# Performance work log

Hardware: AMD Instinct MI355X
Metric: run time of the kernel (lower is better)

Reference implementation:

```python
import jax, jax.numpy as jnp
import numpy as np

D_MODEL = 32
D_INNER = 64
D_STATE = 16
D_CONV = 4
DT_RANK = 2  # ceil(d_model/16)
ADJUST = 0.5
EPS = 1e-5


def _conv2d(x, w, b, pad):
    y = jax.lax.conv_general_dilated(x, w, (1, 1), [(pad, pad), (pad, pad)],
                                     dimension_numbers=('NCHW', 'OIHW', 'NCHW'))
    return y + b[None, :, None, None]


def _bn(x, g, be, m, v):
    # eval-mode BatchNorm2d
    return (x - m[None, :, None, None]) / jnp.sqrt(v + EPS)[None, :, None, None] \
        * g[None, :, None, None] + be[None, :, None, None]


def _cbr(x, w, b, g, be, m, v, pad):
    return jax.nn.relu(_bn(_conv2d(x, w, b, pad), g, be, m, v))


def _ln_tokens(p, g, b):
    # p: (B,1,H,W); LayerNorm(1) over the singleton channel per token
    B, _, H, W = p.shape
    t = p.reshape(B, 1, H * W).transpose(0, 2, 1)  # (B,N,1)
    mu = t.mean(-1, keepdims=True)
    var = ((t - mu) ** 2).mean(-1, keepdims=True)
    t = (t - mu) / jnp.sqrt(var + EPS) * g + b
    return t.transpose(0, 2, 1).reshape(B, 1, H, W)


def _selective_scan(u, delta, A, Bm, Cm, Dp):
    # u, delta: (B,L,d_inner); Bm, Cm: (B,L,d_state)
    dBu = delta * u
    def step(h, inp):
        d_t, bu_t, B_t, C_t = inp  # (B,di),(B,di),(B,ds),(B,ds)
        dA = jnp.exp(d_t[..., None] * A)        # (B,di,ds)
        h = dA * h + bu_t[..., None] * B_t[:, None, :]
        y = jnp.einsum('bds,bs->bd', h, C_t)
        return h, y
    h0 = jnp.zeros((u.shape[0], D_INNER, D_STATE), u.dtype)
    xs = (delta.transpose(1, 0, 2), dBu.transpose(1, 0, 2),
          Bm.transpose(1, 0, 2), Cm.transpose(1, 0, 2))
    _, ys = jax.lax.scan(step, h0, xs)
    return ys.transpose(1, 0, 2) + u * Dp


def _mamba(tok, in_w, cw, cb, xp_w, dt_w, dt_b, A_log, Dp, out_w):
    # tok: (B,L,d_model)
    xz = tok @ in_w.T                              # (B,L,2*d_inner)
    xm, z = xz[..., :D_INNER], xz[..., D_INNER:]
    # causal depthwise conv1d over sequence
    xc = jax.lax.conv_general_dilated(xm.transpose(0, 2, 1), cw, (1,), [(D_CONV - 1, 0)],
                                      dimension_numbers=('NCH', 'OIH', 'NCH'),
                                      feature_group_count=D_INNER)
    u = jax.nn.silu(xc + cb[None, :, None]).transpose(0, 2, 1)  # (B,L,di)
    xdbl = u @ xp_w.T                              # (B,L,dt_rank+2*d_state)
    dt = xdbl[..., :DT_RANK]
    Bm = xdbl[..., DT_RANK:DT_RANK + D_STATE]
    Cm = xdbl[..., DT_RANK + D_STATE:]
    delta = jax.nn.softplus(dt @ dt_w.T + dt_b)    # (B,L,di)
    A = -jnp.exp(A_log)                            # (di,ds)
    y = _selective_scan(u, delta, A, Bm, Cm, Dp)
    y = y * jax.nn.silu(z)
    return y @ out_w.T


def hpe_forward(x, w7, b7, g1, be1, m1, v1, w3, b3, g2, be2, m2, v2,
                w1, b1, g3, be3, m3, v3,
                in_w, cw, cb, xp_w, dt_w, dt_b, A_log, Dp, out_w,
                w4, b4, g4, be4, m4, v4, p1w, p1b, p2w, p2b, lng, lnb):
    B, C, H, W = x.shape
    x = x.reshape(B, C, H // 2, 2, W // 2, 2).max(axis=(3, 5))  # MaxPool2d(2,2)
    x = _cbr(x, w7, b7, g1, be1, m1, v1, 3)
    x = _cbr(x, w3, b3, g2, be2, m2, v2, 1)
    x = _cbr(x, w1, b1, g3, be3, m3, v3, 0)
    B, C, H, W = x.shape
    p1 = _ln_tokens(_conv2d(x, p1w, p1b, 0), lng, lnb)
    tok = x.reshape(B, C, H * W).transpose(0, 2, 1)  # (B,N,C)
    y = _mamba(tok, in_w, cw, cb, xp_w, dt_w, dt_b, A_log, Dp, out_w)
    x = ADJUST * y.transpose(0, 2, 1).reshape(B, C, H, W) + (1.0 - ADJUST) * x
    p2 = _ln_tokens(_conv2d(x, p2w, p2b, 0), lng, lnb)
    return _cbr(x, w4, b4, g4, be4, m4, v4, 0) + p1 + p2


def setup_inputs() -> dict:
    key = jax.random.key(0)
    ks = jax.random.split(key, 16)
    f32 = jnp.float32
    def nrm(k, s, sc=0.05):
        return jax.random.normal(k, s, dtype=f32) * sc
    C = 32
    d = {}
    d['x'] = jax.random.normal(ks[0], (8, 3, 256, 256), dtype=f32)
    d['w7'] = nrm(ks[1], (C, 3, 7, 7), 0.1); d['b7'] = jnp.zeros(C, f32)
    d['g1'] = jnp.ones(C, f32); d['be1'] = jnp.zeros(C, f32); d['m1'] = jnp.zeros(C, f32); d['v1'] = jnp.ones(C, f32)
    d['w3'] = nrm(ks[2], (C, C, 3, 3), 0.1); d['b3'] = jnp.zeros(C, f32)
    d['g2'] = jnp.ones(C, f32); d['be2'] = jnp.zeros(C, f32); d['m2'] = jnp.zeros(C, f32); d['v2'] = jnp.ones(C, f32)
    d['w1'] = nrm(ks[3], (C, C, 1, 1), 0.2); d['b1'] = jnp.zeros(C, f32)
    d['g3'] = jnp.ones(C, f32); d['be3'] = jnp.zeros(C, f32); d['m3'] = jnp.zeros(C, f32); d['v3'] = jnp.ones(C, f32)
    d['in_w'] = nrm(ks[4], (2 * D_INNER, C), 0.1)
    d['cw'] = nrm(ks[5], (D_INNER, 1, D_CONV), 0.2); d['cb'] = jnp.zeros(D_INNER, f32)
    d['xp_w'] = nrm(ks[6], (DT_RANK + 2 * D_STATE, D_INNER), 0.1)
    d['dt_w'] = nrm(ks[7], (D_INNER, DT_RANK), 0.5)
    d['dt_b'] = jnp.log(jnp.expm1(jnp.linspace(0.001, 0.1, D_INNER, dtype=f32)))
    d['A_log'] = jnp.log(jnp.tile(jnp.arange(1, D_STATE + 1, dtype=f32), (D_INNER, 1)))
    d['Dp'] = jnp.ones(D_INNER, f32)
    d['out_w'] = nrm(ks[8], (C, D_INNER), 0.1)
    d['w4'] = nrm(ks[9], (C, C, 1, 1), 0.2); d['b4'] = jnp.zeros(C, f32)
    d['g4'] = jnp.ones(C, f32); d['be4'] = jnp.zeros(C, f32); d['m4'] = jnp.zeros(C, f32); d['v4'] = jnp.ones(C, f32)
    d['p1w'] = nrm(ks[10], (1, C, 1, 1), 0.2); d['p1b'] = jnp.zeros(1, f32)
    d['p2w'] = nrm(ks[11], (1, C, 1, 1), 0.2); d['p2b'] = jnp.zeros(1, f32)
    d['lng'] = jnp.ones(1, f32); d['lnb'] = nrm(ks[12], (1,), 1.0)
    return d


def reference(x, w7, b7, g1, be1, m1, v1, w3, b3, g2, be2, m2, v2,
              w1, b1, g3, be3, m3, v3,
              in_w, cw, cb, xp_w, dt_w, dt_b, A_log, Dp, out_w,
              w4, b4, g4, be4, m4, v4, p1w, p1b, p2w, p2b, lng, lnb):
    return hpe_forward(x, w7, b7, g1, be1, m1, v1, w3, b3, g2, be2, m2, v2,
                       w1, b1, g3, be3, m3, v3,
                       in_w, cw, cb, xp_w, dt_w, dt_b, A_log, Dp, out_w,
                       w4, b4, g4, be4, m4, v4, p1w, p1b, p2w, p2b, lng, lnb)
```

## Files before the change

### kernel.cpp

```cpp
#include <hip/hip_runtime.h>
#include <hip/hip_bf16.h>

#define B_ 8
#define HP 128
#define WP 128
#define LL 16384
#define NC 512
#define LC 32
#define NSUP 32
#define KSUP 16
#define EPSF 1e-5f
#define LOG2E 1.44269504f

__device__ __forceinline__ float softplusf(float x){
    float ax = fabsf(x);
    float e = exp2f(-LOG2E*ax);
    return fmaxf(x, 0.f) + 0.69314718f*log2f(1.f + e);
}
__device__ __forceinline__ float siluf(float x){
    return x * __builtin_amdgcn_rcpf(1.f + exp2f(-LOG2E*x));
}

__global__ void prep_kernel(const float* __restrict__ w7, const float* __restrict__ b7,
                            const float* __restrict__ g1, const float* __restrict__ be1,
                            const float* __restrict__ m1, const float* __restrict__ v1,
                            const float* __restrict__ w3, const float* __restrict__ b3,
                            const float* __restrict__ g2, const float* __restrict__ be2,
                            const float* __restrict__ m2, const float* __restrict__ v2,
                            const float* __restrict__ w1, const float* __restrict__ b1,
                            const float* __restrict__ g3, const float* __restrict__ be3,
                            const float* __restrict__ m3, const float* __restrict__ v3,
                            const float* __restrict__ w4, const float* __restrict__ b4,
                            const float* __restrict__ g4, const float* __restrict__ be4,
                            const float* __restrict__ m4, const float* __restrict__ v4,
                            const float* __restrict__ out_w,
                            float* __restrict__ w7t, float* __restrict__ bf1,
                            float* __restrict__ w3t, float* __restrict__ bf2,
                            float* __restrict__ w1t, float* __restrict__ bf3,
                            float* __restrict__ w4t, float* __restrict__ bf4,
                            float* __restrict__ WcT, float* __restrict__ w4h){
    int tid = threadIdx.x;
    if (tid < 32){
        float s1 = g1[tid]*rsqrtf(v1[tid]+EPSF);
        bf1[tid] = (b7[tid]-m1[tid])*s1 + be1[tid];
        float s2 = g2[tid]*rsqrtf(v2[tid]+EPSF);
        bf2[tid] = (b3[tid]-m2[tid])*s2 + be2[tid];
        float s3 = g3[tid]*rsqrtf(v3[tid]+EPSF);
        bf3[tid] = (b1[tid]-m3[tid])*s3 + be3[tid];
        float s4 = g4[tid]*rsqrtf(v4[tid]+EPSF);
        bf4[tid] = (b4[tid]-m4[tid])*s4 + be4[tid];
    }
    for (int e = tid; e < 147*32; e += blockDim.x){
        int co = e & 31; int r = e >> 5;
        float s = g1[co]*rsqrtf(v1[co]+EPSF);
        w7t[e] = w7[co*147 + r]*s;
    }
    for (int e = tid; e < 288*32; e += blockDim.x){
        int co = e & 31; int r = e >> 5;
        float s = g2[co]*rsqrtf(v2[co]+EPSF);
        w3t[e] = w3[co*288 + r]*s;
    }
    for (int e = tid; e < 32*32; e += blockDim.x){
        int co = e & 31; int ci = e >> 5;
        float s3 = g3[co]*rsqrtf(v3[co]+EPSF);
        w1t[e] = w1[co*32+ci]*s3;
        float s4 = g4[co]*rsqrtf(v4[co]+EPSF);
        w4t[e] = w4[co*32+ci]*s4;
    }
    __syncthreads();
    for (int e = tid; e < 64*32; e += blockDim.x){
        int co = e & 31; int d = e >> 5;
        float a = 0.f;
        for (int c = 0; c < 32; c++) a = fmaf(w4t[c*32+co], out_w[c*64+d], a);
        WcT[d*32+co] = 0.5f*a;
    }
    for (int e = tid; e < 1024; e += blockDim.x) w4h[e] = 0.5f*w4t[e];
}

__global__ __launch_bounds__(256) void pool_kernel(const float* __restrict__ x, float* __restrict__ p){
    int idx = blockIdx.x*256 + threadIdx.x;
    if (idx >= B_*3*HP*WP) return;
    int j = idx & 127; int i = (idx>>7) & 127; int bc = idx >> 14;
    const float* src = x + ((size_t)bc*256 + 2*i)*256 + 2*j;
    float a = src[0], b = src[1], c = src[256], d = src[257];
    p[idx] = fmaxf(fmaxf(a,b), fmaxf(c,d));
}

__global__ __launch_bounds__(256) void conv7_kernel(const float* __restrict__ p, const float* __restrict__ w7t,
                                                    const float* __restrict__ bf1, float* __restrict__ x1){
    __shared__ float lds[3*10*70];
    int tx = threadIdx.x & 63, ty = threadIdx.x >> 6;
    int b = blockIdx.z >> 1, coh = (blockIdx.z & 1) * 16;
    int i0 = blockIdx.y*4, j0 = blockIdx.x*64;
    for (int e = threadIdx.x; e < 3*10*70; e += 256){
        int col = e % 70; int r2 = e / 70; int row = r2 % 10; int ci = r2 / 10;
        int gi = i0 + row - 3, gj = j0 + col - 3;
        float v = 0.f;
        if (gi>=0 && gi<HP && gj>=0 && gj<WP)
            v = p[((b*3+ci)*HP+gi)*WP+gj];
        lds[e] = v;
    }
    __syncthreads();
    float acc[16];
    #pragma unroll
    for (int co=0; co<16; co++) acc[co]=0.f;
    for (int ci=0; ci<3; ci++){
        for (int ky=0; ky<7; ky++){
            #pragma unroll
            for (int kx=0; kx<7; kx++){
                float v = lds[ci*700 + (ty+ky)*70 + tx+kx];
                const float* w = w7t + ((ci*7+ky)*7+kx)*32 + coh;
                #pragma unroll
                for (int co=0; co<16; co++) acc[co] = fmaf(v, w[co], acc[co]);
            }
        }
    }
    size_t base = ((size_t)(b*32)+coh)*LL + (i0+ty)*WP + (j0+tx);
    #pragma unroll
    for (int co=0; co<16; co++)
        x1[base + (size_t)co*LL] = fmaxf(acc[co]+bf1[coh+co], 0.f);
}

__global__ __launch_bounds__(256) void conv31_kernel(const float* __restrict__ x1, const float* __restrict__ w3t,
                                                     const float* __restrict__ bf2, const float* __restrict__ w1t,
                                                     const float* __restrict__ bf3, float* __restrict__ x3){
    __shared__ float lds[16*6*66];
    int tx = threadIdx.x & 63, ty = threadIdx.x >> 6;
    int b = blockIdx.z;
    int i0 = blockIdx.y*4, j0 = blockIdx.x*64;
    float acc[32];
    #pragma unroll
    for (int co=0; co<32; co++) acc[co]=0.f;
    for (int pass=0; pass<2; ++pass){
        int cibase = pass*16;
        for (int e = threadIdx.x; e < 16*6*66; e += 256){
            int col = e % 66; int r2 = e / 66; int row = r2 % 6; int ci = r2 / 6;
            int gi = i0 + row - 1, gj = j0 + col - 1;
            float v = 0.f;
            if (gi>=0 && gi<HP && gj>=0 && gj<WP)
                v = x1[((b*32+cibase+ci)*HP+gi)*WP+gj];
            lds[e] = v;
        }
        __syncthreads();
        for (int ci=0; ci<16; ci++){
            #pragma unroll
            for (int ky=0; ky<3; ky++){
                #pragma unroll
                for (int kx=0; kx<3; kx++){
                    float v = lds[ci*396 + (ty+ky)*66 + tx+kx];
                    const float* w = w3t + (((cibase+ci)*3+ky)*3+kx)*32;
                    #pragma unroll
                    for (int co=0; co<32; co++) acc[co] = fmaf(v, w[co], acc[co]);
                }
            }
        }
        __syncthreads();
    }
    #pragma unroll
    for (int co=0; co<32; co++) acc[co] = fmaxf(acc[co]+bf2[co], 0.f);
    float a3[32];
    #pragma unroll
    for (int co=0; co<32; co++) a3[co] = bf3[co];
    #pragma unroll
    for (int ci=0; ci<32; ci++){
        float v = acc[ci];
        const float* w = w1t + ci*32;
        #pragma unroll
        for (int co=0; co<32; co++) a3[co] = fmaf(v, w[co], a3[co]);
    }
    size_t base = ((size_t)(b*32))*LL + (i0+ty)*WP + (j0+tx);
    #pragma unroll
    for (int co=0; co<32; co++)
        x3[base + (size_t)co*LL] = fmaxf(a3[co], 0.f);
}

__global__ __launch_bounds__(256) void inproj_dw_kernel(const float* __restrict__ x3, const float* __restrict__ in_w,
                                                        const float* __restrict__ cw, const float* __restrict__ cb,
                                                        const float* __restrict__ xp_w,
                                                        float* __restrict__ Z, float* __restrict__ U,
                                                        float* __restrict__ BC, float* __restrict__ CC,
                                                        float* __restrict__ DT){
    __shared__ float xmL[67*65];
    __shared__ float buf[64*65];
    int lane = threadIdx.x & 63;
    int wv = __builtin_amdgcn_readfirstlane(threadIdx.x >> 6);
    int b = blockIdx.x >> 8;
    int t0 = (blockIdx.x & 255) * 64;
    size_t gbase = (size_t)b*LL + t0;

    float xvm[32], xvz[32];
    int tm = t0 - 3 + lane;
    #pragma unroll
    for (int c=0;c<32;c++)
        xvm[c] = (tm >= 0) ? x3[((size_t)(b*32+c))*LL + tm] : 0.f;
    #pragma unroll
    for (int c=0;c<32;c++)
        xvz[c] = x3[((size_t)(b*32+c))*LL + t0 + lane];

    for (int kk=0; kk<16; ++kk){
        int k = wv*16 + kk;
        const float* wxp = in_w + k*32;
        const float* wzp = in_w + (64+k)*32;
        float am = 0.f, az = 0.f;
        #pragma unroll
        for (int c=0;c<32;c++){
            am = fmaf(xvm[c], wxp[c], am);
            az = fmaf(xvz[c], wzp[c], az);
        }
        xmL[lane*65 + k] = am;
        buf[lane*65 + k] = az;
        if (lane >= 61){
            float am2 = 0.f;
            #pragma unroll
            for (int c=0;c<32;c++) am2 = fmaf(xvz[c], wxp[c], am2);
            xmL[(lane+3)*65 + k] = am2;
        }
    }
    __syncthreads();
    for (int i=0;i<16;i++){
        int tt = wv*16 + i;
        Z[(gbase + tt)*64 + lane] = buf[tt*65 + lane];
    }
    __syncthreads();
    for (int kk=0; kk<16; ++kk){
        int k = wv*16 + kk;
        float c0 = cw[k*4], c1 = cw[k*4+1], c2 = cw[k*4+2], c3 = cw[k*4+3];
        float a = cb[k];
        a = fmaf(c0, xmL[(lane+0)*65 + k], a);
        a = fmaf(c1, xmL[(lane+1)*65 + k], a);
        a = fmaf(c2, xmL[(lane+2)*65 + k], a);
        a = fmaf(c3, xmL[(lane+3)*65 + k], a);
        buf[lane*65 + k] = siluf(a);
    }
    __syncthreads();
    for (int i=0;i<16;i++){
        int tt = wv*16 + i;
        U[(gbase + tt)*64 + lane] = buf[tt*65 + lane];
    }
    {
        float* oT = xmL;
        const float* urow = &buf[lane*65];
        float a[9];
        #pragma unroll
        for (int jj=0;jj<9;jj++) a[jj]=0.f;
        #pragma unroll
        for (int dc=0; dc<4; ++dc){
            float uv[16];
            #pragma unroll
            for (int i=0;i<16;i++) uv[i] = urow[dc*16+i];
            #pragma unroll
            for (int jj=0;jj<9;jj++){
                int j = wv*9+jj; if (j>33) j=33;
                const float* w = xp_w + j*64 + dc*16;
                float s = 0.f;
                #pragma unroll
                for (int i=0;i<16;i++) s = fmaf(uv[i], w[i], s);
                a[jj] += s;
            }
        }
        #pragma unroll
        for (int jj=0;jj<9;jj++){
            int j = wv*9+jj;
            if (j < 34) oT[lane*35 + j] = a[jj];
        }
    }
    __syncthreads();
    {
        const float* oT = xmL;
        int e = threadIdx.x;
        if (e < 128){
            int tk = e >> 1, j = e & 1;
            DT[(gbase + tk)*2 + j] = oT[tk*35 + j];
        }
        for (int it=0; it<4; ++it){
            int e2 = threadIdx.x + it*256;
            int tk = e2 >> 4, j = e2 & 15;
            BC[(gbase + tk)*16 + j] = oT[tk*35 + 2 + j];
            CC[(gbase + tk)*16 + j] = oT[tk*35 + 18 + j];
        }
    }
}

__global__ __launch_bounds__(256) void scan1_kernel(const float* __restrict__ DT, const float* __restrict__ U,
                                                    const float* __restrict__ BC,
                                                    const float* __restrict__ dt_w, const float* __restrict__ dt_b,
                                                    const float* __restrict__ A_log,
                                                    float* __restrict__ HEND, float* __restrict__ SDL){
    int d = threadIdx.x & 63; int cq = threadIdx.x >> 6;
    int b = blockIdx.x >> 7; int c = ((blockIdx.x & 127) << 2) | cq;
    float A2_0 = -__expf(A_log[d*16])*LOG2E;
    float w0 = dt_w[d*2], w1 = dt_w[d*2+1], bD = dt_b[d];
    float h[16];
    #pragma unroll
    for (int s=0;s<16;s++) h[s]=0.f;
    float sd = 0.f;
    size_t tbase = (size_t)b*LL + c*LC;
    const float2* dtp = (const float2*)(DT + tbase*2);
    const float* up = U + tbase*64 + d;
    const float4* bp = (const float4*)(BC + tbase*16);
    for (int tt=0; tt<LC; ++tt){
        float2 dv = dtp[tt];
        float delta = softplusf(fmaf(dv.x, w0, fmaf(dv.y, w1, bD)));
        float uv = up[(size_t)tt*64];
        float du = delta*uv;
        float4 B0 = bp[tt*4+0], B1 = bp[tt*4+1], B2 = bp[tt*4+2], B3 = bp[tt*4+3];
        float bb[16] = {B0.x,B0.y,B0.z,B0.w, B1.x,B1.y,B1.z,B1.w,
                        B2.x,B2.y,B2.z,B2.w, B3.x,B3.y,B3.z,B3.w};
        float a1 = exp2f(delta*A2_0);
        float a2=a1*a1, a3=a2*a1, a4=a2*a2;
        float a8=a4*a4, a12=a8*a4, a16=a8*a8;
        float rr[16] = {a1,a2,a3,a4, a4*a1,a4*a2,a4*a3,a8,
                        a8*a1,a8*a2,a8*a3,a12, a12*a1,a12*a2,a12*a3,a16};
        #pragma unroll
        for (int s=0;s<16;s++)
            h[s] = fmaf(rr[s], h[s], du*bb[s]);
        sd += delta;
    }
    float4* hp = (float4*)(HEND + (((size_t)(b*NC)+c)*64 + d)*16);
    hp[0] = make_float4(h[0],h[1],h[2],h[3]);
    hp[1] = make_float4(h[4],h[5],h[6],h[7]);
    hp[2] = make_float4(h[8],h[9],h[10],h[11]);
    hp[3] = make_float4(h[12],h[13],h[14],h[15]);
    SDL[((size_t)(b*NC)+c)*64 + d] = sd;
}

__global__ __launch_bounds__(256) void scan2a_kernel(const float* __restrict__ HEND, const float* __restrict__ SDL,
                                                     const float* __restrict__ A_log,
                                                     float* __restrict__ HSUP, float* __restrict__ SDS){
    int tid = blockIdx.x*256 + threadIdx.x;
    int s = tid & 15; int d = (tid>>4) & 63; int g = (tid>>10) & 31; int b = tid >> 15;
    float A2 = -__expf(A_log[d*16+s])*LOG2E;
    float H = 0.f, sds = 0.f;
    #pragma unroll 4
    for (int k=0; k<KSUP; ++k){
        int c = g*KSUP + k;
        size_t ci = ((size_t)(b*NC)+c)*64 + d;
        float sv = SDL[ci];
        H = fmaf(exp2f(A2*sv), H, HEND[ci*16+s]);
        sds += sv;
    }
    HSUP[tid] = H;
    if (s == 0) SDS[(b*NSUP+g)*64 + d] = sds;
}

__global__ __launch_bounds__(256) void scan2b_kernel(float* __restrict__ HSUP, const float* __restrict__ SDS,
                                                     const float* __restrict__ A_log){
    int tid = blockIdx.x*256 + threadIdx.x;
    if (tid >= B_*64*16) return;
    int s = tid & 15; int d = (tid>>4) & 63; int b = tid >> 10;
    float A2 = -__expf(A_log[d*16+s])*LOG2E;
    float H = 0.f;
    for (int g=0; g<NSUP; ++g){
        size_t idx = ((((size_t)b*NSUP+g)*64 + d)*16) + s;
        float tmp = HSUP[idx];
        HSUP[idx] = H;
        H = fmaf(exp2f(A2*SDS[(b*NSUP+g)*64 + d]), H, tmp);
    }
}

__global__ __launch_bounds__(256) void scan2c_kernel(float* __restrict__ HEND, const float* __restrict__ SDL,
                                                     const float* __restrict__ A_log,
                                                     const float* __restrict__ HSUP){
    int tid = blockIdx.x*256 + threadIdx.x;
    int s = tid & 15; int d = (tid>>4) & 63; int g = (tid>>10) & 31; int b = tid >> 15;
    float A2 = -__expf(A_log[d*16+s])*LOG2E;
    float H = HSUP[tid];
    #pragma unroll 4
    for (int k=0; k<KSUP; ++k){
        int c = g*KSUP + k;
        size_t ci = ((size_t)(b*NC)+c)*64 + d;
        float tmp = HEND[ci*16+s];
        HEND[ci*16+s] = H;
        H = fmaf(exp2f(A2*SDL[ci]), H, tmp);
    }
}

__global__ __launch_bounds__(256) void scan3_kernel(const float* __restrict__ DT, const float* __restrict__ U,
                                                    const float* __restrict__ BC, const float* __restrict__ CC,
                                                    const float* __restrict__ dt_w, const float* __restrict__ dt_b,
                                                    const float* __restrict__ A_log, const float* __restrict__ Dp,
                                                    const float* __restrict__ HST, const float* __restrict__ Z,
                                                    const float* __restrict__ WcT, const float* __restrict__ w4h,
                                                    const float* __restrict__ x3, const float* __restrict__ bf4,
                                                    const float* __restrict__ lnb, float* __restrict__ out){
    __shared__ float yT[128*65];
    __shared__ float wl[97*32];
    int d = threadIdx.x & 63; int cq = threadIdx.x >> 6;
    int b = blockIdx.x >> 7; int cbase4 = (blockIdx.x & 127) << 2;
    int c = cbase4 | cq;
    for (int e = threadIdx.x; e < 3072; e += 256)
        wl[e] = (e < 2048) ? WcT[e] : w4h[e-2048];
    if (threadIdx.x < 32) wl[3072+threadIdx.x] = bf4[threadIdx.x];
    int tok = threadIdx.x & 127;
    int hf  = threadIdx.x >> 7;
    size_t tcol = (size_t)cbase4*LC + tok;
    float x3v[32];
    #pragma unroll
    for (int c2=0;c2<32;c2++) x3v[c2] = x3[((size_t)(b*32+c2))*LL + tcol];

    float A2_0 = -__expf(A_log[d*16])*LOG2E;
    float w0 = dt_w[d*2], w1 = dt_w[d*2+1], bD = dt_b[d];
    float Dd = Dp[d];
    float h[16];
    const float4* hp = (const float4*)(HST + (((size_t)(b*NC)+c)*64 + d)*16);
    #pragma unroll
    for (int q=0;q<4;q++){
        float4 f = hp[q];
        h[q*4]=f.x; h[q*4+1]=f.y; h[q*4+2]=f.z; h[q*4+3]=f.w;
    }
    size_t tbase = (size_t)b*LL + c*LC;
    const float2* dtp = (const float2*)(DT + tbase*2);
    const float* up = U + tbase*64 + d;
    const float4* bp = (const float4*)(BC + tbase*16);
    const float4* cp = (const float4*)(CC + tbase*16);
    const float* zp = Z + tbase*64 + d;
    for (int tt=0; tt<LC; ++tt){
        float2 dv = dtp[tt];
        float delta = softplusf(fmaf(dv.x, w0, fmaf(dv.y, w1, bD)));
        float uv = up[(size_t)tt*64];
        float du = delta*uv;
        float4 B0 = bp[tt*4+0], B1 = bp[tt*4+1], B2 = bp[tt*4+2], B3 = bp[tt*4+3];
        float4 C0 = cp[tt*4+0], C1 = cp[tt*4+1], C2 = cp[tt*4+2], C3 = cp[tt*4+3];
        float bb[16] = {B0.x,B0.y,B0.z,B0.w, B1.x,B1.y,B1.z,B1.w,
                        B2.x,B2.y,B2.z,B2.w, B3.x,B3.y,B3.z,B3.w};
        float cc[16] = {C0.x,C0.y,C0.z,C0.w, C1.x,C1.y,C1.z,C1.w,
                        C2.x,C2.y,C2.z,C2.w, C3.x,C3.y,C3.z,C3.w};
        float a1 = exp2f(delta*A2_0);
        float a2=a1*a1, a3=a2*a1, a4=a2*a2;
        float a8=a4*a4, a12=a8*a4, a16=a8*a8;
        float rr[16] = {a1,a2,a3,a4, a4*a1,a4*a2,a4*a3,a8,
                        a8*a1,a8*a2,a8*a3,a12, a12*a1,a12*a2,a12*a3,a16};
        float y0=0.f, y1=0.f, y2=0.f, y3=0.f;
        #pragma unroll
        for (int s=0;s<4;s++){
            h[s]    = fmaf(rr[s],    h[s],    du*bb[s]);
            h[s+4]  = fmaf(rr[s+4],  h[s+4],  du*bb[s+4]);
            h[s+8]  = fmaf(rr[s+8],  h[s+8],  du*bb[s+8]);
            h[s+12] = fmaf(rr[s+12], h[s+12], du*bb[s+12]);
            y0 = fmaf(h[s],    cc[s],    y0);
            y1 = fmaf(h[s+4],  cc[s+4],  y1);
            y2 = fmaf(h[s+8],  cc[s+8],  y2);
            y3 = fmaf(h[s+12], cc[s+12], y3);
        }
        float y = (y0+y1)+(y2+y3);
        float zv = zp[(size_t)tt*64];
        float yy = fmaf(uv, Dd, y);
        yT[(cq*LC + tt)*65 + d] = yy * siluf(zv);
    }
    __syncthreads();
    int cob = hf*16;
    const float* yrow = &yT[tok*65];
    float acc[16];
    #pragma unroll
    for (int o=0;o<16;o++) acc[o] = wl[3072+cob+o];
    #pragma unroll
    for (int dc=0; dc<4; ++dc){
        float uv[16];
        #pragma unroll
        for (int i=0;i<16;i++) uv[i] = yrow[dc*16+i];
        #pragma unroll
        for (int i=0;i<16;i++){
            const float* w = &wl[(dc*16+i)*32 + cob];
            float v = uv[i];
            #pragma unroll
            for (int o=0;o<16;o++) acc[o] = fmaf(v, w[o], acc[o]);
        }
    }
    #pragma unroll
    for (int c2=0; c2<32; ++c2){
        float v = x3v[c2];
        const float* w = &wl[(64+c2)*32 + cob];
        #pragma unroll
        for (int o=0;o<16;o++) acc[o] = fmaf(v, w[o], acc[o]);
    }
    float add2 = 2.f*lnb[0];
    #pragma unroll
    for (int o=0;o<16;o++)
        out[((size_t)(b*32)+cob+o)*LL + tcol] = fmaxf(acc[o], 0.f) + add2;
}

extern "C" void kernel_launch(void* const* d_in, const int* in_sizes, int n_in,
                              void* d_out, int out_size, void* d_ws, size_t ws_size,
                              hipStream_t stream) {
    const float* x    = (const float*)d_in[0];
    const float* w7   = (const float*)d_in[1];
    const float* b7   = (const float*)d_in[2];
    const float* g1   = (const float*)d_in[3];
    const float* be1  = (const float*)d_in[4];
    const float* m1   = (const float*)d_in[5];
    const float* v1   = (const float*)d_in[6];
    const float* w3   = (const float*)d_in[7];
    const float* b3   = (const float*)d_in[8];
    const float* g2   = (const float*)d_in[9];
    const float* be2  = (const float*)d_in[10];
    const float* m2   = (const float*)d_in[11];
    const float* v2   = (const float*)d_in[12];
    const float* w1   = (const float*)d_in[13];
    const float* b1   = (const float*)d_in[14];
    const float* g3   = (const float*)d_in[15];
    const float* be3  = (const float*)d_in[16];
    const float* m3   = (const float*)d_in[17];
    const float* v3   = (const float*)d_in[18];
    const float* in_w = (const float*)d_in[19];
    const float* cw   = (const float*)d_in[20];
    const float* cb   = (const float*)d_in[21];
    const float* xp_w = (const float*)d_in[22];
    const float* dt_w = (const float*)d_in[23];
    const float* dt_b = (const float*)d_in[24];
    const float* A_log= (const float*)d_in[25];
    const float* Dp   = (const float*)d_in[26];
    const float* out_w= (const float*)d_in[27];
    const float* w4   = (const float*)d_in[28];
    const float* b4   = (const float*)d_in[29];
    const float* g4   = (const float*)d_in[30];
    const float* be4  = (const float*)d_in[31];
    const float* m4   = (const float*)d_in[32];
    const float* v4   = (const float*)d_in[33];
    const float* lnb  = (const float*)d_in[39];

    float* ws = (float*)d_ws;
    size_t OFF_POOL = 0;
    size_t OFF_Z    = 393216;
    size_t OFF_X1   = OFF_Z;
    size_t OFF_X3   = OFF_Z + 8388608;
    size_t OFF_U    = OFF_X3 + 4194304;
    size_t OFF_BC   = OFF_U + 8388608;
    size_t OFF_CC   = OFF_BC + 2097152;
    size_t OFF_HE   = OFF_CC + 2097152;
    size_t OFF_DT   = OFF_HE + 4194304;
    size_t OFF_HSUP = OFF_DT + 262144;
    size_t OFF_SDS  = OFF_HSUP + 262144;
    size_t OFF_W    = OFF_SDS + 16384;
    float* w7t = ws + OFF_W;
    float* w3t = w7t + 4704;
    float* w1t = w3t + 9216;
    float* w4t = w1t + 1024;
    float* bf1 = w4t + 1024;
    float* bf2 = bf1 + 32;
    float* bf3 = bf2 + 32;
    float* bf4 = bf3 + 32;
    float* WcT = bf4 + 32;
    float* w4h = WcT + 2048;
    float* SDL = ws + OFF_POOL;

    prep_kernel<<<1, 512, 0, stream>>>(w7,b7,g1,be1,m1,v1, w3,b3,g2,be2,m2,v2,
                                       w1,b1,g3,be3,m3,v3, w4,b4,g4,be4,m4,v4, out_w,
                                       w7t,bf1,w3t,bf2,w1t,bf3,w4t,bf4, WcT,w4h);
    pool_kernel<<<1536, 256, 0, stream>>>(x, ws+OFF_POOL);
    conv7_kernel<<<dim3(2,32,16), 256, 0, stream>>>(ws+OFF_POOL, w7t, bf1, ws+OFF_X1);
    conv31_kernel<<<dim3(2,32,8), 256, 0, stream>>>(ws+OFF_X1, w3t, bf2, w1t, bf3, ws+OFF_X3);
    inproj_dw_kernel<<<2048, 256, 0, stream>>>(ws+OFF_X3, in_w, cw, cb, xp_w,
                                               ws+OFF_Z, ws+OFF_U, ws+OFF_BC, ws+OFF_CC, ws+OFF_DT);
    scan1_kernel<<<1024, 256, 0, stream>>>(ws+OFF_DT, ws+OFF_U, ws+OFF_BC, dt_w, dt_b, A_log,
                                           ws+OFF_HE, SDL);
    scan2a_kernel<<<1024, 256, 0, stream>>>(ws+OFF_HE, SDL, A_log, ws+OFF_HSUP, ws+OFF_SDS);
    scan2b_kernel<<<32, 256, 0, stream>>>(ws+OFF_HSUP, ws+OFF_SDS, A_log);
    scan2c_kernel<<<1024, 256, 0, stream>>>(ws+OFF_HE, SDL, A_log, ws+OFF_HSUP);
    scan3_kernel<<<1024, 256, 0, stream>>>(ws+OFF_DT, ws+OFF_U, ws+OFF_BC, ws+OFF_CC, dt_w, dt_b,
                                           A_log, Dp, ws+OFF_HE, ws+OFF_Z,
                                           WcT, w4h, ws+OFF_X3, bf4, lnb, (float*)d_out);
}
```

Before: 295.0 us.

## Fuse chunk-local scan pass into in-projection kernel and drop scan3 weight staging

Runs the first chunk-local selective-scan pass (per-chunk end state and summed delta) inside the in-projection kernel. It reads DT, B and U straight from shared memory, which removes a separate launch and the global re-read of DT, U and BC. The shared tile is re-laid-out to a stride of 36 so B can be read as float4. The output-projection stage of scan3 no longer stages weights in LDS and no longer preloads x3; it reads them from global memory through the cache. Only 128 of 256 threads do the serial scan work, which lengthens the in-projection kernel's tail.

```diff
diff --git a/kernel.cpp b/kernel.cpp
--- a/kernel.cpp
+++ b/kernel.cpp
@@ -177,9 +177,12 @@
 __global__ __launch_bounds__(256) void inproj_dw_kernel(const float* __restrict__ x3, const float* __restrict__ in_w,
                                                         const float* __restrict__ cw, const float* __restrict__ cb,
                                                         const float* __restrict__ xp_w,
+                                                        const float* __restrict__ dt_w, const float* __restrict__ dt_b,
+                                                        const float* __restrict__ A_log,
                                                         float* __restrict__ Z, float* __restrict__ U,
                                                         float* __restrict__ BC, float* __restrict__ CC,
-                                                        float* __restrict__ DT){
+                                                        float* __restrict__ DT,
+                                                        float* __restrict__ HEND, float* __restrict__ SDL){
     __shared__ float xmL[67*65];
     __shared__ float buf[64*65];
     int lane = threadIdx.x & 63;
@@ -261,7 +264,10 @@
         #pragma unroll
         for (int jj=0;jj<9;jj++){
             int j = wv*9+jj;
-            if (j < 34) oT[lane*35 + j] = a[jj];
+            if (j < 34){
+                int col = (j < 2) ? (32+j) : (j-2);
+                oT[lane*36 + col] = a[jj];
+            }
         }
     }
     __syncthreads();
@@ -270,58 +276,52 @@
         int e = threadIdx.x;
         if (e < 128){
             int tk = e >> 1, j = e & 1;
-            DT[(gbase + tk)*2 + j] = oT[tk*35 + j];
+            DT[(gbase + tk)*2 + j] = oT[tk*36 + 32 + j];
         }
         for (int it=0; it<4; ++it){
             int e2 = threadIdx.x + it*256;
             int tk = e2 >> 4, j = e2 & 15;
-            BC[(gbase + tk)*16 + j] = oT[tk*35 + 2 + j];
-            CC[(gbase + tk)*16 + j] = oT[tk*35 + 18 + j];
-        }
-    }
-}
-
-__global__ __launch_bounds__(256) void scan1_kernel(const float* __restrict__ DT, const float* __restrict__ U,
-                                                    const float* __restrict__ BC,
-                                                    const float* __restrict__ dt_w, const float* __restrict__ dt_b,
-                                                    const float* __restrict__ A_log,
-                                                    float* __restrict__ HEND, float* __restrict__ SDL){
-    int d = threadIdx.x & 63; int cq = threadIdx.x >> 6;
-    int b = blockIdx.x >> 7; int c = ((blockIdx.x & 127) << 2) | cq;
-    float A2_0 = -__expf(A_log[d*16])*LOG2E;
-    float w0 = dt_w[d*2], w1 = dt_w[d*2+1], bD = dt_b[d];
-    float h[16];
-    #pragma unroll
-    for (int s=0;s<16;s++) h[s]=0.f;
-    float sd = 0.f;
-    size_t tbase = (size_t)b*LL + c*LC;
-    const float2* dtp = (const float2*)(DT + tbase*2);
-    const float* up = U + tbase*64 + d;
-    const float4* bp = (const float4*)(BC + tbase*16);
-    for (int tt=0; tt<LC; ++tt){
-        float2 dv = dtp[tt];
-        float delta = softplusf(fmaf(dv.x, w0, fmaf(dv.y, w1, bD)));
-        float uv = up[(size_t)tt*64];
-        float du = delta*uv;
-        float4 B0 = bp[tt*4+0], B1 = bp[tt*4+1], B2 = bp[tt*4+2], B3 = bp[tt*4+3];
-        float bb[16] = {B0.x,B0.y,B0.z,B0.w, B1.x,B1.y,B1.z,B1.w,
-                        B2.x,B2.y,B2.z,B2.w, B3.x,B3.y,B3.z,B3.w};
-        float a1 = exp2f(delta*A2_0);
-        float a2=a1*a1, a3=a2*a1, a4=a2*a2;
-        float a8=a4*a4, a12=a8*a4, a16=a8*a8;
-        float rr[16] = {a1,a2,a3,a4, a4*a1,a4*a2,a4*a3,a8,
-                        a8*a1,a8*a2,a8*a3,a12, a12*a1,a12*a2,a12*a3,a16};
-        #pragma unroll
-        for (int s=0;s<16;s++)
-            h[s] = fmaf(rr[s], h[s], du*bb[s]);
-        sd += delta;
-    }
-    float4* hp = (float4*)(HEND + (((size_t)(b*NC)+c)*64 + d)*16);
-    hp[0] = make_float4(h[0],h[1],h[2],h[3]);
-    hp[1] = make_float4(h[4],h[5],h[6],h[7]);
-    hp[2] = make_float4(h[8],h[9],h[10],h[11]);
-    hp[3] = make_float4(h[12],h[13],h[14],h[15]);
-    SDL[((size_t)(b*NC)+c)*64 + d] = sd;
+            BC[(gbase + tk)*16 + j] = oT[tk*36 + j];
+            CC[(gbase + tk)*16 + j] = oT[tk*36 + 16 + j];
+        }
+    }
+    if (threadIdx.x < 128){
+        int d = threadIdx.x & 63; int cq = threadIdx.x >> 6;
+        int c = (blockIdx.x & 255)*2 + cq;
+        const float* oT = xmL;
+        float A2_0 = -__expf(A_log[d*16])*LOG2E;
+        float w0 = dt_w[d*2], w1 = dt_w[d*2+1], bD = dt_b[d];
+        float h[16];
+        #pragma unroll
+        for (int s=0;s<16;s++) h[s]=0.f;
+        float sd = 0.f;
+        for (int tt=0; tt<LC; ++tt){
+            int tok = cq*LC + tt;
+            float dt0 = oT[tok*36+32], dt1 = oT[tok*36+33];
+            float delta = softplusf(fmaf(dt0, w0, fmaf(dt1, w1, bD)));
+            float uv = buf[tok*65 + d];
+            float du = delta*uv;
+            const float4* brow = (const float4*)&oT[tok*36];
+            float4 B0 = brow[0], B1 = brow[1], B2 = brow[2], B3 = brow[3];
+            float bb[16] = {B0.x,B0.y,B0.z,B0.w, B1.x,B1.y,B1.z,B1.w,
+                            B2.x,B2.y,B2.z,B2.w, B3.x,B3.y,B3.z,B3.w};
+            float a1 = exp2f(delta*A2_0);
+            float a2=a1*a1, a3=a2*a1, a4=a2*a2;
+            float a8=a4*a4, a12=a8*a4, a16=a8*a8;
+            float rr[16] = {a1,a2,a3,a4, a4*a1,a4*a2,a4*a3,a8,
+                            a8*a1,a8*a2,a8*a3,a12, a12*a1,a12*a2,a12*a3,a16};
+            #pragma unroll
+            for (int s=0;s<16;s++)
+                h[s] = fmaf(rr[s], h[s], du*bb[s]);
+            sd += delta;
+        }
+        float4* hp = (float4*)(HEND + (((size_t)(b*NC)+c)*64 + d)*16);
+        hp[0] = make_float4(h[0],h[1],h[2],h[3]);
+        hp[1] = make_float4(h[4],h[5],h[6],h[7]);
+        hp[2] = make_float4(h[8],h[9],h[10],h[11]);
+        hp[3] = make_float4(h[12],h[13],h[14],h[15]);
+        SDL[((size_t)(b*NC)+c)*64 + d] = sd;
+    }
 }
 
 __global__ __launch_bounds__(256) void scan2a_kernel(const float* __restrict__ HEND, const float* __restrict__ SDL,
@@ -384,20 +384,9 @@
                                                     const float* __restrict__ x3, const float* __restrict__ bf4,
                                                     const float* __restrict__ lnb, float* __restrict__ out){
     __shared__ float yT[128*65];
-    __shared__ float wl[97*32];
     int d = threadIdx.x & 63; int cq = threadIdx.x >> 6;
     int b = blockIdx.x >> 7; int cbase4 = (blockIdx.x & 127) << 2;
     int c = cbase4 | cq;
-    for (int e = threadIdx.x; e < 3072; e += 256)
-        wl[e] = (e < 2048) ? WcT[e] : w4h[e-2048];
-    if (threadIdx.x < 32) wl[3072+threadIdx.x] = bf4[threadIdx.x];
-    int tok = threadIdx.x & 127;
-    int hf  = threadIdx.x >> 7;
-    size_t tcol = (size_t)cbase4*LC + tok;
-    float x3v[32];
-    #pragma unroll
-    for (int c2=0;c2<32;c2++) x3v[c2] = x3[((size_t)(b*32+c2))*LL + tcol];
-
     float A2_0 = -__expf(A_log[d*16])*LOG2E;
     float w0 = dt_w[d*2], w1 = dt_w[d*2+1], bD = dt_b[d];
     float Dd = Dp[d];
@@ -448,11 +437,14 @@
         yT[(cq*LC + tt)*65 + d] = yy * siluf(zv);
     }
     __syncthreads();
+    int tok = threadIdx.x & 127;
+    int hf  = threadIdx.x >> 7;
     int cob = hf*16;
+    size_t tcol = (size_t)cbase4*LC + tok;
     const float* yrow = &yT[tok*65];
     float acc[16];
     #pragma unroll
-    for (int o=0;o<16;o++) acc[o] = wl[3072+cob+o];
+    for (int o=0;o<16;o++) acc[o] = bf4[cob+o];
     #pragma unroll
     for (int dc=0; dc<4; ++dc){
         float uv[16];
@@ -460,7 +452,7 @@
         for (int i=0;i<16;i++) uv[i] = yrow[dc*16+i];
         #pragma unroll
         for (int i=0;i<16;i++){
-            const float* w = &wl[(dc*16+i)*32 + cob];
+            const float* w = WcT + (dc*16+i)*32 + cob;
             float v = uv[i];
             #pragma unroll
             for (int o=0;o<16;o++) acc[o] = fmaf(v, w[o], acc[o]);
@@ -468,8 +460,8 @@
     }
     #pragma unroll
     for (int c2=0; c2<32; ++c2){
-        float v = x3v[c2];
-        const float* w = &wl[(64+c2)*32 + cob];
+        float v = x3[((size_t)(b*32+c2))*LL + tcol];
+        const float* w = w4h + c2*32 + cob;
         #pragma unroll
         for (int o=0;o<16;o++) acc[o] = fmaf(v, w[o], acc[o]);
     }
@@ -549,10 +541,9 @@
     pool_kernel<<<1536, 256, 0, stream>>>(x, ws+OFF_POOL);
     conv7_kernel<<<dim3(2,32,16), 256, 0, stream>>>(ws+OFF_POOL, w7t, bf1, ws+OFF_X1);
     conv31_kernel<<<dim3(2,32,8), 256, 0, stream>>>(ws+OFF_X1, w3t, bf2, w1t, bf3, ws+OFF_X3);
-    inproj_dw_kernel<<<2048, 256, 0, stream>>>(ws+OFF_X3, in_w, cw, cb, xp_w,
-                                               ws+OFF_Z, ws+OFF_U, ws+OFF_BC, ws+OFF_CC, ws+OFF_DT);
-    scan1_kernel<<<1024, 256, 0, stream>>>(ws+OFF_DT, ws+OFF_U, ws+OFF_BC, dt_w, dt_b, A_log,
-                                           ws+OFF_HE, SDL);
+    inproj_dw_kernel<<<2048, 256, 0, stream>>>(ws+OFF_X3, in_w, cw, cb, xp_w, dt_w, dt_b, A_log,
+                                               ws+OFF_Z, ws+OFF_U, ws+OFF_BC, ws+OFF_CC, ws+OFF_DT,
+                                               ws+OFF_HE, SDL);
     scan2a_kernel<<<1024, 256, 0, stream>>>(ws+OFF_HE, SDL, A_log, ws+OFF_HSUP, ws+OFF_SDS);
     scan2b_kernel<<<32, 256, 0, stream>>>(ws+OFF_HSUP, ws+OFF_SDS, A_log);
     scan2c_kernel<<<1024, 256, 0, stream>>>(ws+OFF_HE, SDL, A_log, ws+OFF_HSUP);
```

Result: no change. 293.3 us (-0.6%).
